# Optimization experiments

Hardware: AMD Instinct MI355X
Metric: run time of the kernel (lower is better)

The kernel has to match this reference:

```python
import jax, jax.numpy as jnp
import numpy as np

SIZES = (1, 2, 4, 8)
C_IN = 64
KC = C_IN // 8      # key_channels = out_channels // 8 = 8
VC = C_IN           # value_channels = out_channels = 64
N_STAGES = len(SIZES)


def setup_inputs() -> dict:
    key = jax.random.key(0)
    ks = jax.random.split(key, 16)
    N, C, H, W = 1, C_IN, 64, 64
    inp = {
        "x1": jax.random.normal(ks[0], (N, C, H, W), jnp.float32),
        "x2": jax.random.normal(ks[1], (N, C, H, W), jnp.float32),
        # per-stage 1x1 conv weights (stacked over the 4 PAM stages)
        "Wq": jax.random.normal(ks[2], (N_STAGES, KC, C), jnp.float32) * 0.02,
        "bq": jnp.zeros((N_STAGES, KC), jnp.float32),
        "gammaq": 1.0 + jax.random.normal(ks[3], (N_STAGES, KC), jnp.float32) * 0.02,
        "betaq": jnp.zeros((N_STAGES, KC), jnp.float32),
        "Wk": jax.random.normal(ks[4], (N_STAGES, KC, C), jnp.float32) * 0.02,
        "bk": jnp.zeros((N_STAGES, KC), jnp.float32),
        "gammak": 1.0 + jax.random.normal(ks[5], (N_STAGES, KC), jnp.float32) * 0.02,
        "betak": jnp.zeros((N_STAGES, KC), jnp.float32),
        "Wv": jax.random.normal(ks[6], (N_STAGES, VC, C), jnp.float32) * 0.02,
        "bv": jnp.zeros((N_STAGES, VC), jnp.float32),
        # final 1x1 conv: in = C * n_stages, out = C, no bias
        "Wo": jax.random.normal(ks[7], (C, VC * N_STAGES), jnp.float32) * 0.02,
    }
    return inp


def _pam_block(x, Wq, bq, gq, betq, Wk, bk, gk, betk, Wv, bv, scale):
    # x: [N, C, H, 2W] (two images concatenated along width)
    N, C, H, W2 = x.shape
    w = W2 // 2
    kc = Wq.shape[0]

    def proj(W, b):  # 1x1 conv
        return jnp.einsum('nchw,kc->nkhw', x, W) + b[:, None, None]

    # BatchNorm (inference form: zero running mean / unit variance) folded to affine
    q = gq[:, None, None] * proj(Wq, bq) + betq[:, None, None]
    k = gk[:, None, None] * proj(Wk, bk) + betk[:, None, None]
    v = proj(Wv, bv)

    hl, wl = H // scale, w // scale

    def to_blocks(t):
        ch = t.shape[1]
        # stack left/right halves on a trailing axis: [N, ch, H, w, 2]
        t = jnp.stack([t[..., :w], t[..., w:]], axis=-1)
        # split into scale x scale spatial blocks -> [N, s*s, ch, hl*wl*2]
        t = t.reshape(N, ch, scale, hl, scale, wl, 2)
        t = t.transpose(0, 2, 4, 1, 3, 5, 6)
        return t.reshape(N, scale * scale, ch, hl * wl * 2)

    qb, kb, vb = to_blocks(q), to_blocks(k), to_blocks(v)

    sim = jnp.einsum('nbkp,nbkq->nbpq', qb, kb) * (kc ** -0.5)
    att = jax.nn.softmax(sim, axis=-1)
    # context = V @ att^T : ctx[c,p] = sum_q v[c,q] * att[p,q]
    ctx = jnp.einsum('nbcq,nbpq->nbcp', vb, att)

    Cv = Wv.shape[0]
    ctx = ctx.reshape(N, scale, scale, Cv, hl, wl, 2)
    ctx = ctx.transpose(0, 3, 1, 4, 2, 5, 6).reshape(N, Cv, H, w, 2)
    # re-concatenate the two halves along width -> [N, Cv, H, 2w]
    return jnp.concatenate([ctx[..., 0], ctx[..., 1]], axis=3)


def reference(x1, x2, Wq, bq, gammaq, betaq, Wk, bk, gammak, betak, Wv, bv, Wo):
    h_w = x1.shape[3]
    x = jnp.concatenate([x1, x2], axis=3)  # [N, C, H, 2W]
    priors = [
        _pam_block(x, Wq[i], bq[i], gammaq[i], betaq[i],
                   Wk[i], bk[i], gammak[i], betak[i],
                   Wv[i], bv[i], SIZES[i])
        for i in range(N_STAGES)
    ]
    cat = jnp.concatenate(priors, axis=1)  # [N, 4C, H, 2W]
    out = jnp.einsum('ndhw,od->nohw', cat, Wo)  # final 1x1 conv, no bias
    return out[:, :, :, :h_w], out[:, :, :, h_w:]


if __name__ == '__main__':
    o1, o2 = reference(**setup_inputs())
    print(o1.shape, o2.shape)
```

## Files before the change

### kernel.cpp

```cpp
#include <hip/hip_runtime.h>


typedef _Float16 f16x8 __attribute__((ext_vector_type(8)));
typedef float f32x16 __attribute__((ext_vector_type(16)));
typedef short bf16x8 __attribute__((ext_vector_type(8)));

__device__ __forceinline__ unsigned short f2bf(float f){
    union{float f;unsigned int i;}v; v.f=f;
    unsigned int r = v.i + 0x7fffu + ((v.i>>16)&1u);
    return (unsigned short)(r>>16);
}
__device__ __forceinline__ unsigned short f2h(float f){
    union{_Float16 h; unsigned short u;}v; v.h = (_Float16)f; return v.u;
}
__device__ __forceinline__ unsigned pack2h(float a, float b){
    auto pk = __builtin_amdgcn_cvt_pkrtz(a, b);
    unsigned u; __builtin_memcpy(&u, &pk, 4); return u;
}
__device__ __forceinline__ float exp2fast(float x){ return __builtin_amdgcn_exp2f(x); }
__device__ __forceinline__ int rfl(int x){ return __builtin_amdgcn_readfirstlane(x); }

#define QMUL 0.5100697233f

__global__ __launch_bounds__(256) void proj_all_kernel(
    const float* __restrict__ x1, const float* __restrict__ x2,
    const float* __restrict__ Wq, const float* __restrict__ bq,
    const float* __restrict__ gq, const float* __restrict__ beq,
    const float* __restrict__ Wk, const float* __restrict__ bk,
    const float* __restrict__ gk, const float* __restrict__ bek,
    const float* __restrict__ Wv, const float* __restrict__ bv,
    unsigned short* __restrict__ Qb, unsigned short* __restrict__ Kb,
    unsigned short* __restrict__ Vf)
{
    __shared__ __align__(16) float xs[64][68];
    __shared__ __align__(16) unsigned vqk[64][8];
    __shared__ __align__(16) unsigned short vv[64][64];

    const int wg = blockIdx.x, st = wg >> 8, rr = wg & 255;
    const int chunk = rr >> 1, cgrp = rr & 1;
    const int lgP = 13 - 2*st, Pm1 = (1<<lgP) - 1;
    const int hb = 6 - st, wlm = (1<<hb) - 1;
    const int t = threadIdx.x;
    const int gp0 = chunk*64;
    const int blk = gp0 >> lgP, p0 = gp0 & Pm1;
    const int si = blk >> st, sj = blk & ((1<<st)-1);
    const int hwbase = ((si<<hb)<<6) | (sj<<hb);

    for (int idx = t; idx < 4096; idx += 256) {
        int c = idx >> 6, g = idx & 63;
        int p = p0 + g, half = p & 1, pw = p >> 1;
        int hw = hwbase | ((pw>>hb)<<6) | (pw & wlm);
        xs[g][c] = (half ? x2 : x1)[c*4096 + hw];
    }
    __syncthreads();

    const int px = t & 63, wv = t >> 6;
    float xr[64];
    #pragma unroll
    for (int q4 = 0; q4 < 16; ++q4)
        *(float4*)&xr[q4*4] = *(const float4*)&xs[px][q4*4];

#define VRANGE(LO,HI)                                              \
    for (int ch = (LO); ch < (HI); ++ch) {                         \
        const int cu = rfl(st*64 + ch);                            \
        const float* wp = Wv + cu*64;                              \
        float d = bv[cu];                                          \
        _Pragma("unroll")                                          \
        for (int k = 0; k < 64; ++k) d += wp[k]*xr[k];             \
        vv[ch][px] = f2h(d);                                       \
    }
#define KPROJ(CH,DST)                                              \
    {   const int cu = rfl(st*8 + (CH));                           \
        const float* wp = Wk + cu*64;                              \
        float d = 0.f;                                             \
        _Pragma("unroll")                                          \
        for (int k = 0; k < 64; ++k) d += wp[k]*xr[k];             \
        float gm = gk[cu];                                         \
        (DST) = gm*(d + bk[cu]) + bek[cu]; }

    if (cgrp == 0) {
        if (wv == 0) {
            float qv8[8];
            for (int ch = 0; ch < 8; ++ch) {
                const int cu = rfl(st*8 + ch);
                const float* wp = Wq + cu*64;
                float d = 0.f;
                #pragma unroll
                for (int k = 0; k < 64; ++k) d += wp[k]*xr[k];
                float gm = gq[cu];
                qv8[ch] = (gm*(d + bq[cu]) + beq[cu])*QMUL;
            }
            #pragma unroll
            for (int i = 0; i < 4; ++i) vqk[px][i] = pack2h(qv8[2*i], qv8[2*i+1]);
            float k0v, k1v; KPROJ(0, k0v) KPROJ(1, k1v)
            vqk[px][4] = pack2h(k0v, k1v);
        } else if (wv == 1) {
            float ka, kb2;
            KPROJ(2, ka) KPROJ(3, kb2) vqk[px][5] = pack2h(ka, kb2);
            KPROJ(4, ka) KPROJ(5, kb2) vqk[px][6] = pack2h(ka, kb2);
            KPROJ(6, ka) KPROJ(7, kb2) vqk[px][7] = pack2h(ka, kb2);
            VRANGE(0, 4)
        } else if (wv == 2) { VRANGE(4, 14) }
        else               { VRANGE(14, 24) }
    } else {
        if      (wv == 0) { VRANGE(24, 34) }
        else if (wv == 1) { VRANGE(34, 44) }
        else if (wv == 2) { VRANGE(44, 54) }
        else              { VRANGE(54, 64) }
    }
#undef VRANGE
#undef KPROJ
    __syncthreads();

    unsigned short* Vst = Vf + st*524288 + (blk << (lgP+6));
    if (cgrp == 0) {
        if (t < 64) {
            *(uint4*)(Qb + st*65536 + (gp0 + t)*8) = *(const uint4*)&vqk[t][0];
        } else if (t < 128) {
            int p2 = t - 64;
            *(uint4*)(Kb + st*65536 + (gp0 + p2)*8) = *(const uint4*)&vqk[p2][4];
        }
        if (t < 192) {
            int ch = t >> 3, o = t & 7;
            unsigned short tmp[8];
            #pragma unroll
            for (int u = 0; u < 8; ++u) {
                int s = o*8 + u;
                tmp[u] = vv[ch][((s&1)<<5) | (s>>1)];
            }
            *(uint4*)(Vst + (ch << lgP) + p0 + o*8) = *(const uint4*)tmp;
        }
    } else {
        for (int task = t; task < 320; task += 256) {
            int ch = 24 + (task >> 3), o = task & 7;
            unsigned short tmp[8];
            #pragma unroll
            for (int u = 0; u < 8; ++u) {
                int s = o*8 + u;
                tmp[u] = vv[ch][((s&1)<<5) | (s>>1)];
            }
            *(uint4*)(Vst + (ch << lgP) + p0 + o*8) = *(const uint4*)tmp;
        }
    }
}

__global__ __launch_bounds__(256) void attn_kernel(
    const unsigned short* __restrict__ Qb, const unsigned short* __restrict__ Kb,
    const unsigned short* __restrict__ Vf,
    float* __restrict__ PART, float* __restrict__ LPART)
{
    __shared__ __align__(16) unsigned short Ps[4][2432];

    const int wg = blockIdx.x;
    const int t = threadIdx.x, lane = t & 63, wv = t >> 6;
    const int l31 = lane & 31, lhi = lane >> 5;

    int st, qt, slot, kbase, nkw;
    if (wg < 512)       { st=0; qt=wg>>1;  slot=wg&1;
                          kbase=(wg&1)*4096 + wv*1024; nkw=1024; }
    else if (wg < 1024) { int r=wg-512;  st=1; qt=r>>1; slot=2+(r&1);
                          kbase=(r&1)*1024 + wv*256;  nkw=256; }
    else if (wg < 1280) { st=2; qt=wg-1024; slot=4; kbase=wv*128; nkw=128; }
    else                { st=3; qt=wg-1280; slot=5; kbase=wv*64;
                          nkw=(wv<2)?64:0; }

    const int lgP = 13 - 2*st, P = 1 << lgP;
    const int blk = qt >> (lgP - 5);
    const int q0  = (qt & ((P>>5)-1)) * 32;

    const unsigned short* Qg = Qb + st*65536 + blk*P*8;
    const unsigned short* Kg = Kb + st*65536 + blk*P*8;
    const unsigned short* Vg = Vf + st*524288 + blk*P*64;

    f16x8 qa;
    #pragma unroll
    for (int j = 0; j < 8; ++j) qa[j] = (_Float16)0.f;
    if (lane < 32) qa = *(const f16x8*)(Qg + (q0 + l31)*8);

    f32x16 acc0, acc1;
    #pragma unroll
    for (int r = 0; r < 16; ++r) { acc0[r] = 0.f; acc1[r] = 0.f; }
    float rowsum[16];
    #pragma unroll
    for (int r = 0; r < 16; ++r) rowsum[r] = 0.f;

    unsigned short* Pw = Ps[wv];
    unsigned* Pw32 = (unsigned*)Pw;
    for (int k0 = kbase; k0 < kbase + nkw; k0 += 64) {
        f16x8 kb0 = *(const f16x8*)(Kg + (k0 + l31)*8);
        f16x8 kb1 = *(const f16x8*)(Kg + (k0 + 32 + l31)*8);
        f32x16 S0, S1;
        #pragma unroll
        for (int r = 0; r < 16; ++r) { S0[r] = 0.f; S1[r] = 0.f; }
        S0 = __builtin_amdgcn_mfma_f32_32x32x16_f16(qa, kb0, S0, 0, 0, 0);
        S1 = __builtin_amdgcn_mfma_f32_32x32x16_f16(qa, kb1, S1, 0, 0, 0);

        #pragma unroll
        for (int r = 0; r < 16; ++r) {
            float p0 = exp2fast(S0[r]);
            float p1 = exp2fast(S1[r]);
            rowsum[r] += p0 + p1;
            int qrow = (r&3) + 8*(r>>2) + 4*lhi;
            Pw32[qrow*38 + l31] = pack2h(p0, p1);
        }

        #pragma unroll
        for (int kc = 0; kc < 4; ++kc) {
            f16x8 pa  = *(const f16x8*)(Pw + l31*76 + kc*16 + 8*lhi);
            const int ko = k0 + kc*16 + 8*lhi;
            f16x8 vb0 = *(const f16x8*)(Vg + l31*P + ko);
            f16x8 vb1 = *(const f16x8*)(Vg + (32 + l31)*P + ko);
            acc0 = __builtin_amdgcn_mfma_f32_32x32x16_f16(pa, vb0, acc0, 0, 0, 0);
            acc1 = __builtin_amdgcn_mfma_f32_32x32x16_f16(pa, vb1, acc1, 0, 0, 0);
        }
    }

    float* SC = (float*)Pw;
    #pragma unroll
    for (int r = 0; r < 16; ++r) {
        int qrow = (r&3) + 8*(r>>2) + 4*lhi;
        SC[qrow*33 + l31] = rowsum[r];
    }
    float lsum_reg = 0.f;
    if (lane < 32) {
        #pragma unroll 8
        for (int j = 0; j < 32; ++j) lsum_reg += SC[l31*33 + j];
    }

    float* B0 = (float*)&Ps[0][0];
    float* B1 = B0 + 2048;
    float* Lm = B0 + 4096;
    __syncthreads();
    if (wv == 0 || wv == 2) {
        float* B = (wv == 0) ? B0 : B1;
        #pragma unroll
        for (int r = 0; r < 16; ++r) {
            int qrow = (r&3) + 8*(r>>2) + 4*lhi;
            B[qrow*64 + l31]      = acc0[r];
            B[qrow*64 + 32 + l31] = acc1[r];
        }
        if (lane < 32) Lm[(wv>>1)*32 + l31] = lsum_reg;
    }
    __syncthreads();
    if (wv == 1 || wv == 3) {
        float* B = (wv == 1) ? B0 : B1;
        #pragma unroll
        for (int r = 0; r < 16; ++r) {
            int qrow = (r&3) + 8*(r>>2) + 4*lhi;
            B[qrow*64 + l31]      += acc0[r];
            B[qrow*64 + 32 + l31] += acc1[r];
        }
        if (lane < 32) Lm[(wv>>1)*32 + l31] += lsum_reg;
    }
    __syncthreads();

    float4* Pslab4 = (float4*)(PART + slot*524288 + qt*2048);
    const float4* B04 = (const float4*)B0;
    const float4* B14 = (const float4*)B1;
    #pragma unroll
    for (int r = 0; r < 2; ++r) {
        int idx = t + r*256;
        float4 a = B04[idx], b = B14[idx];
        Pslab4[idx] = float4{a.x+b.x, a.y+b.y, a.z+b.z, a.w+b.w};
    }
    if (t < 32)
        LPART[slot*8192 + qt*32 + t] = Lm[t] + Lm[32 + t];
}

__global__ __launch_bounds__(256) void normconv_kernel(
    const float* __restrict__ PART, const float* __restrict__ LPART,
    const float* __restrict__ Wo, float* __restrict__ out)
{
    __shared__ __align__(16) unsigned short csb[32][264];
    __shared__ __align__(16) unsigned short wof[16384];
    __shared__ float voutf[64][33];
    __shared__ float linv[4][32];
    __shared__ int gpar[4][32];
    const int t = threadIdx.x;
    const int px0 = blockIdx.x * 32;

    {
        int oc = t >> 2, d0 = (t & 3) * 64;
        for (int b = 0; b < 8; ++b) {
            int d = d0 + b*8;
            float4 w0 = *(const float4*)(Wo + oc*256 + d);
            float4 w1 = *(const float4*)(Wo + oc*256 + d + 4);
            unsigned short tmp[8];
            tmp[0]=f2bf(w0.x); tmp[1]=f2bf(w0.y); tmp[2]=f2bf(w0.z); tmp[3]=f2bf(w0.w);
            tmp[4]=f2bf(w1.x); tmp[5]=f2bf(w1.y); tmp[6]=f2bf(w1.z); tmp[7]=f2bf(w1.w);
            *(uint4*)&wof[(d>>3)*512 + oc*8] = *(const uint4*)tmp;
        }
    }
    if (t < 128) {
        const int s0tab[4] = {0,2,4,5};
        const int sctab[4] = {2,2,1,1};
        int stt = t >> 5, i = t & 31;
        int pix = px0 + i;
        int half = pix >> 12, hw = pix & 4095;
        int h = hw >> 6, w = hw & 63;
        int hb = 6 - stt, wlm = (1<<hb)-1;
        int si = h >> hb, sj = w >> hb, hi = h & wlm, wi = w & wlm;
        int blk = (si << stt) | sj;
        int p = (((hi << hb) | wi) << 1) | half;
        int gp = blk*(8192>>(2*stt)) + p;
        gpar[stt][i] = gp;
        int s0 = s0tab[stt];
        float l = LPART[s0*8192 + gp];
        if (sctab[stt] == 2) l += LPART[(s0+1)*8192 + gp];
        linv[stt][i] = 1.f / l;
    }
    __syncthreads();

    {
        const int s0tab[4] = {0,2,4,5};
        int gpx = t >> 3, cvg = (t & 7) * 8;
        for (int stt = 0; stt < 4; ++stt) {
            int gp = gpar[stt][gpx];
            const float* p = PART + s0tab[stt]*524288
                           + (gp>>5)*2048 + (gp&31)*64 + cvg;
            float4 a = *(const float4*)p;
            float4 b = *(const float4*)(p + 4);
            if (stt < 2) {
                float4 a2 = *(const float4*)(p + 524288);
                float4 b2 = *(const float4*)(p + 524288 + 4);
                a.x+=a2.x; a.y+=a2.y; a.z+=a2.z; a.w+=a2.w;
                b.x+=b2.x; b.y+=b2.y; b.z+=b2.z; b.w+=b2.w;
            }
            float li = linv[stt][gpx];
            unsigned short tmp[8];
            tmp[0]=f2bf(a.x*li); tmp[1]=f2bf(a.y*li); tmp[2]=f2bf(a.z*li); tmp[3]=f2bf(a.w*li);
            tmp[4]=f2bf(b.x*li); tmp[5]=f2bf(b.y*li); tmp[6]=f2bf(b.z*li); tmp[7]=f2bf(b.w*li);
            *(uint4*)&csb[gpx][stt*64 + cvg] = *(const uint4*)tmp;
        }
    }
    __syncthreads();

    const int lane = t & 63, wvv = t >> 6;
    const int l31 = lane & 31, lhi = lane >> 5;
    const int nh = wvv & 1, kh = wvv >> 1;
    f32x16 acc;
    #pragma unroll
    for (int r = 0; r < 16; ++r) acc[r] = 0.f;
    #pragma unroll
    for (int s = 0; s < 8; ++s) {
        int dg = kh*16 + s*2 + lhi;
        bf16x8 a = *(const bf16x8*)&csb[l31][kh*128 + s*16 + 8*lhi];
        bf16x8 b = *(const bf16x8*)&wof[dg*512 + (nh*32 + l31)*8];
        acc = __builtin_amdgcn_mfma_f32_32x32x16_bf16(a, b, acc, 0, 0, 0);
    }
    if (kh == 0) {
        #pragma unroll
        for (int r = 0; r < 16; ++r)
            voutf[nh*32 + l31][(r&3) + 8*(r>>2) + 4*lhi] = acc[r];
    }
    __syncthreads();
    if (kh == 1) {
        #pragma unroll
        for (int r = 0; r < 16; ++r)
            voutf[nh*32 + l31][(r&3) + 8*(r>>2) + 4*lhi] += acc[r];
    }
    __syncthreads();

    const int half = px0 >> 12, hw0 = px0 & 4095;
    float* obase = out + half*262144 + hw0;
    #pragma unroll
    for (int r = 0; r < 8; ++r) {
        int idx = t + r*256;
        int oc = idx >> 5, pxi = idx & 31;
        obase[oc*4096 + pxi] = voutf[oc][pxi];
    }
}

extern "C" void kernel_launch(void* const* d_in, const int* in_sizes, int n_in,
                              void* d_out, int out_size, void* d_ws, size_t ws_size,
                              hipStream_t stream)
{
    (void)out_size; (void)ws_size;
    const float *x1, *x2, *Wq, *bq, *gq, *beq, *Wk, *bk, *gk, *bek, *Wv, *bv, *Wo;

    if (n_in >= 13 && in_sizes[0] == 2048) {
        Wk  = (const float*)d_in[0];  Wo  = (const float*)d_in[1];
        Wq  = (const float*)d_in[2];  Wv  = (const float*)d_in[3];
        bek = (const float*)d_in[4];  beq = (const float*)d_in[5];
        bk  = (const float*)d_in[6];  bq  = (const float*)d_in[7];
        bv  = (const float*)d_in[8];  gk  = (const float*)d_in[9];
        gq  = (const float*)d_in[10];
        x1  = (const float*)d_in[11]; x2  = (const float*)d_in[12];
    } else {
        x1  = (const float*)d_in[0];  x2  = (const float*)d_in[1];
        Wq  = (const float*)d_in[2];  bq  = (const float*)d_in[3];
        gq  = (const float*)d_in[4];  beq = (const float*)d_in[5];
        Wk  = (const float*)d_in[6];  bk  = (const float*)d_in[7];
        gk  = (const float*)d_in[8];  bek = (const float*)d_in[9];
        Wv  = (const float*)d_in[10]; bv  = (const float*)d_in[11];
        Wo  = (const float*)d_in[12];
    }

    unsigned short* Qb = (unsigned short*)d_ws;
    unsigned short* Kb = Qb + 262144;
    unsigned short* Vf = Kb + 262144;
    float* PART  = (float*)d_ws + 1310720;
    float* LPART = PART + 3145728;

    proj_all_kernel<<<1024, 256, 0, stream>>>(x1,x2,Wq,bq,gq,beq,Wk,bk,gk,bek,Wv,bv,Qb,Kb,Vf);
    attn_kernel<<<1536, 256, 0, stream>>>(Qb,Kb,Vf,PART,LPART);
    normconv_kernel<<<256, 256, 0, stream>>>(PART, LPART, Wo, (float*)d_out);
}
```

Before: 156.5 us.

## Store V in MFMA fragment order and split attention keys over eight waves

```diff
diff --git a/kernel.cpp b/kernel.cpp
--- a/kernel.cpp
+++ b/kernel.cpp
@@ -121,35 +121,38 @@
             *(uint4*)(Kb + st*65536 + (gp0 + p2)*8) = *(const uint4*)&vqk[p2][4];
         }
         if (t < 192) {
-            int ch = t >> 3, o = t & 7;
+            int ch = t >> 3, q = t & 7;
+            int kb = q >> 1, lhi = q & 1;
             unsigned short tmp[8];
             #pragma unroll
             for (int u = 0; u < 8; ++u) {
-                int s = o*8 + u;
+                int s = q*8 + u;
                 tmp[u] = vv[ch][((s&1)<<5) | (s>>1)];
             }
-            *(uint4*)(Vst + (ch << lgP) + p0 + o*8) = *(const uint4*)tmp;
+            *(uint4*)(Vst + p0*64 + kb*1024 + (lhi*32 + ch)*8) = *(const uint4*)tmp;
         }
     } else {
         for (int task = t; task < 320; task += 256) {
-            int ch = 24 + (task >> 3), o = task & 7;
+            int ch = 24 + (task >> 3), q = task & 7;
+            int kb = q >> 1, lhi = q & 1;
+            int b = (ch >= 32) ? 1 : 0, l31 = ch & 31;
             unsigned short tmp[8];
             #pragma unroll
             for (int u = 0; u < 8; ++u) {
-                int s = o*8 + u;
+                int s = q*8 + u;
                 tmp[u] = vv[ch][((s&1)<<5) | (s>>1)];
             }
-            *(uint4*)(Vst + (ch << lgP) + p0 + o*8) = *(const uint4*)tmp;
-        }
-    }
-}
-
-__global__ __launch_bounds__(256) void attn_kernel(
+            *(uint4*)(Vst + p0*64 + kb*1024 + b*512 + (lhi*32 + l31)*8) = *(const uint4*)tmp;
+        }
+    }
+}
+
+__global__ __launch_bounds__(512) void attn_kernel(
     const unsigned short* __restrict__ Qb, const unsigned short* __restrict__ Kb,
     const unsigned short* __restrict__ Vf,
     float* __restrict__ PART, float* __restrict__ LPART)
 {
-    __shared__ __align__(16) unsigned short Ps[4][2432];
+    __shared__ __align__(16) unsigned short Ps[8][2432];
 
     const int wg = blockIdx.x;
     const int t = threadIdx.x, lane = t & 63, wv = t >> 6;
@@ -157,10 +160,10 @@
 
     int st, qt, slot, kbase, nkw;
     if (wg < 512)       { st=0; qt=wg>>1;  slot=wg&1;
-                          kbase=(wg&1)*4096 + wv*1024; nkw=1024; }
+                          kbase=(wg&1)*4096 + wv*512; nkw=512; }
     else if (wg < 1024) { int r=wg-512;  st=1; qt=r>>1; slot=2+(r&1);
-                          kbase=(r&1)*1024 + wv*256;  nkw=256; }
-    else if (wg < 1280) { st=2; qt=wg-1024; slot=4; kbase=wv*128; nkw=128; }
+                          kbase=(r&1)*1024 + wv*128;  nkw=128; }
+    else if (wg < 1280) { st=2; qt=wg-1024; slot=4; kbase=wv*64; nkw=64; }
     else                { st=3; qt=wg-1280; slot=5; kbase=wv*64;
                           nkw=(wv<2)?64:0; }
 
@@ -207,9 +210,9 @@
         #pragma unroll
         for (int kc = 0; kc < 4; ++kc) {
             f16x8 pa  = *(const f16x8*)(Pw + l31*76 + kc*16 + 8*lhi);
-            const int ko = k0 + kc*16 + 8*lhi;
-            f16x8 vb0 = *(const f16x8*)(Vg + l31*P + ko);
-            f16x8 vb1 = *(const f16x8*)(Vg + (32 + l31)*P + ko);
+            const unsigned short* vbase = Vg + (k0 + kc*16)*64;
+            f16x8 vb0 = *(const f16x8*)(vbase + lane*8);
+            f16x8 vb1 = *(const f16x8*)(vbase + 512 + lane*8);
             acc0 = __builtin_amdgcn_mfma_f32_32x32x16_f16(pa, vb0, acc0, 0, 0, 0);
             acc1 = __builtin_amdgcn_mfma_f32_32x32x16_f16(pa, vb1, acc1, 0, 0, 0);
         }
@@ -227,44 +230,41 @@
         for (int j = 0; j < 32; ++j) lsum_reg += SC[l31*33 + j];
     }
 
-    float* B0 = (float*)&Ps[0][0];
-    float* B1 = B0 + 2048;
-    float* Lm = B0 + 4096;
-    __syncthreads();
-    if (wv == 0 || wv == 2) {
-        float* B = (wv == 0) ? B0 : B1;
+    float* BB = (float*)&Ps[0][0];
+    float* Lm = BB + 8192;
+    __syncthreads();
+    if (wv < 4) {
+        float* B = BB + wv*2048;
         #pragma unroll
         for (int r = 0; r < 16; ++r) {
             int qrow = (r&3) + 8*(r>>2) + 4*lhi;
             B[qrow*64 + l31]      = acc0[r];
             B[qrow*64 + 32 + l31] = acc1[r];
         }
-        if (lane < 32) Lm[(wv>>1)*32 + l31] = lsum_reg;
-    }
-    __syncthreads();
-    if (wv == 1 || wv == 3) {
-        float* B = (wv == 1) ? B0 : B1;
+        if (lane < 32) Lm[wv*32 + l31] = lsum_reg;
+    }
+    __syncthreads();
+    if (wv >= 4) {
+        float* B = BB + (wv-4)*2048;
         #pragma unroll
         for (int r = 0; r < 16; ++r) {
             int qrow = (r&3) + 8*(r>>2) + 4*lhi;
             B[qrow*64 + l31]      += acc0[r];
             B[qrow*64 + 32 + l31] += acc1[r];
         }
-        if (lane < 32) Lm[(wv>>1)*32 + l31] += lsum_reg;
+        if (lane < 32) Lm[(wv-4)*32 + l31] += lsum_reg;
     }
     __syncthreads();
 
     float4* Pslab4 = (float4*)(PART + slot*524288 + qt*2048);
-    const float4* B04 = (const float4*)B0;
-    const float4* B14 = (const float4*)B1;
-    #pragma unroll
-    for (int r = 0; r < 2; ++r) {
-        int idx = t + r*256;
-        float4 a = B04[idx], b = B14[idx];
-        Pslab4[idx] = float4{a.x+b.x, a.y+b.y, a.z+b.z, a.w+b.w};
+    const float4* B4 = (const float4*)BB;
+    {
+        float4 a = B4[t], b = B4[t+512], c = B4[t+1024], d = B4[t+1536];
+        Pslab4[t] = float4{a.x+b.x+c.x+d.x, a.y+b.y+c.y+d.y,
+                           a.z+b.z+c.z+d.z, a.w+b.w+c.w+d.w};
     }
     if (t < 32)
-        LPART[slot*8192 + qt*32 + t] = Lm[t] + Lm[32 + t];
+        LPART[slot*8192 + qt*32 + t] = Lm[t] + Lm[32+t] + Lm[64+t] + Lm[96+t];
 }
 
 __global__ __launch_bounds__(256) void normconv_kernel(
@@ -403,6 +403,6 @@
     float* LPART = PART + 3145728;
 
     proj_all_kernel<<<1024, 256, 0, stream>>>(x1,x2,Wq,bq,gq,beq,Wk,bk,gk,bek,Wv,bv,Qb,Kb,Vf);
-    attn_kernel<<<1536, 256, 0, stream>>>(Qb,Kb,Vf,PART,LPART);
+    attn_kernel<<<1536, 512, 0, stream>>>(Qb,Kb,Vf,PART,LPART);
     normconv_kernel<<<256, 256, 0, stream>>>(PART, LPART, Wo, (float*)d_out);
 }
```

Result: faster. 147.8 us (-5.5%).
